# Performance work log

Measured on AMD Instinct MI355X. Metric: run time of the kernel, lower is better.

Reference implementation:

```python
import jax, jax.numpy as jnp
import numpy as np

# ---- constants (from init_kwargs / Config) ----
C = 10            # number of classes
P = 128           # fixed prototype capacity per class (masked)
GAMMA = 0.1
B_CONST = 10.0    # b
TAO = 1.0
BETA = 1.0
LAMBDA = 0.1
THRESHOLD = 40.0
EPS = 1e-6        # nn.PairwiseDistance eps (added to the difference)


def setup_inputs() -> dict:
    key = jax.random.key(0)
    k1, k2 = jax.random.split(key)
    features = jax.random.normal(k1, (8192, 512), dtype=jnp.float32)
    labels = jax.random.randint(k2, (8192,), 0, C, dtype=jnp.int32)
    return {"features": features, "labels": labels}


def _assign_prototypes(features, labels):
    """Sequential prototype assignment (faithful to assign_prototype).
    Fixed-capacity store: protos [C,P,D], counts [C,P], nproto [C]."""
    D = features.shape[1]
    protos = jnp.zeros((C, P, D), features.dtype)
    counts = jnp.zeros((C, P), jnp.int32)
    nproto = jnp.zeros((C,), jnp.int32)

    def step(carry, xs):
        protos, counts, nproto = carry
        f, l = xs
        row = protos[l]                       # [P, D]
        cnt = counts[l]                       # [P]
        n = nproto[l]
        valid = jnp.arange(P) < n
        d2 = jnp.sum((f[None, :] - row + EPS) ** 2, axis=-1)
        d2m = jnp.where(valid, d2, jnp.inf)
        idx = jnp.argmin(d2m)
        dmin = jnp.sqrt(d2m[idx])
        do_update = (n > 0) & (dmin < THRESHOLD)
        # running-mean update of closest prototype
        c = cnt[idx].astype(f.dtype)
        new_val = (row[idx] * c + f) / (c + 1.0)
        app_idx = jnp.minimum(n, P - 1)       # append slot (clamped; never hit with these settings)
        tgt_idx = jnp.where(do_update, idx, app_idx)
        tgt_val = jnp.where(do_update, new_val, f)
        tgt_cnt = jnp.where(do_update, cnt[idx] + 1, 1)
        row = row.at[tgt_idx].set(tgt_val)
        cnt = cnt.at[tgt_idx].set(tgt_cnt)
        n = jnp.where(do_update, n, jnp.minimum(n + 1, P))
        protos = protos.at[l].set(row)
        counts = counts.at[l].set(cnt)
        nproto = nproto.at[l].set(n)
        return (protos, counts, nproto), None

    (protos, counts, nproto), _ = jax.lax.scan(step, (protos, counts, nproto), (features, labels))
    return protos, nproto


def _forward(features, labels):
    # assign_prototype uses tensor(features).detach() -> stop_gradient
    protos, nproto = _assign_prototypes(jax.lax.stop_gradient(features), labels)
    B, D = features.shape
    flat = protos.reshape(C * P, D)
    valid = (jnp.arange(P)[None, :] < nproto[:, None]).reshape(C * P)

    # squared PairwiseDistance with eps added to the difference:
    # sum((f - p + eps)^2) = |f|^2 + |p|^2 - 2 f.p + 2*eps*(sum f - sum p) + D*eps^2
    f2 = jnp.sum(features ** 2, axis=-1)          # [B]
    p2 = jnp.sum(flat ** 2, axis=-1)              # [C*P]
    sf = jnp.sum(features, axis=-1)
    sp = jnp.sum(flat, axis=-1)
    d2 = (f2[:, None] + p2[None, :] - 2.0 * (features @ flat.T)
          + 2.0 * EPS * (sf[:, None] - sp[None, :]) + D * EPS * EPS)
    d2 = jnp.maximum(d2, 0.0)                     # [B, C*P]

    # dce loss: probability = 1e-6 + sum_label exp(-g d^2) / sum_all exp(-g d^2)
    expv = jnp.where(valid[None, :], jnp.exp(-GAMMA * d2), 0.0)
    per_class = expv.reshape(B, C, P).sum(-1)     # [B, C]
    one = per_class.sum(-1)                       # [B]
    num = jnp.take_along_axis(per_class, labels[:, None].astype(jnp.int32), axis=1)[:, 0]
    prob = 1e-6 + jnp.where(one > 0.0, num / one, one)
    dce_loss = jnp.sum(-jnp.log(prob))

    # pairwise loss: per sample, per existing class, min distance
    d2c = jnp.where(valid[None, :], d2, jnp.inf).reshape(B, C, P).min(-1)
    dmin = jnp.sqrt(d2c)                          # [B, C]
    sign = jnp.where(labels[:, None] == jnp.arange(C)[None, :], 1.0, -1.0)
    z = B_CONST - (TAO - dmin) * sign
    g = jnp.where(z > 10.0, z, jax.nn.softplus(BETA * z) / BETA)
    exists = nproto > 0                           # only classes present in all_prototypes
    pw_loss = jnp.sum(jnp.where(exists[None, :], g, 0.0))

    return dce_loss + LAMBDA * pw_loss


def reference(features, labels):
    return _forward(features, labels)
```

## Files before the change

### kernel.cpp

```cpp
#include <hip/hip_runtime.h>
#include <math.h>

#define NC 10
#define NP 128
#define ND 512
#define GAMMA  0.1f
#define BCONST 10.0f
#define TAO    1.0f
#define LAMBDA 0.1f
#define THR2   1600.0f
#define FEPS   1e-6f
#define NLDS   12
#define CH     16
#define WPB    4
#define NBLK   131

__device__ __forceinline__ float allredf(float v) {
#pragma unroll
  for (int m = 1; m < 64; m <<= 1) v += __shfl_xor(v, m, 64);
  return v;
}

__global__ __launch_bounds__(256)
void sumc_kernel(const float* __restrict__ feats, const int* __restrict__ labels, int B,
                 float* __restrict__ chunksum, int* __restrict__ order_g,
                 int* __restrict__ cb_g, int* __restrict__ cc_g, int* __restrict__ chb_g,
                 int* __restrict__ ncht_g, int* __restrict__ done_g,
                 int* __restrict__ fail_g, int* __restrict__ nproto_g,
                 float* __restrict__ out)
{
  __shared__ unsigned int lab32[2048];
  __shared__ int list[8192];
  __shared__ int wtot[4][NC];
  __shared__ int cb_s[NC], cc_s[NC], chb_s[NC];
  __shared__ int nchtot_s;

  const int t = threadIdx.x, lane = t & 63, w = t >> 6;

  const int4* lp = (const int4*)labels;
  for (int i = t; i < (B >> 2); i += 256) {
    int4 v = lp[i];
    lab32[i] = (unsigned)(v.x & 255) | ((unsigned)(v.y & 255) << 8)
             | ((unsigned)(v.z & 255) << 16) | ((unsigned)(v.w & 255) << 24);
  }
  __syncthreads();

  const int segsz = (B + 255) >> 8;
  const int i0 = t * segsz, i1 = min(i0 + segsz, B);

  int loc[NC];
#pragma unroll
  for (int c = 0; c < NC; ++c) loc[c] = 0;
  for (int i = i0; i < i1; ++i) {
    int l = (int)((lab32[i >> 2] >> ((i & 3) * 8)) & 255u);
#pragma unroll
    for (int c = 0; c < NC; ++c) loc[c] += (l == c);
  }
  int pre[NC];
#pragma unroll
  for (int c = 0; c < NC; ++c) pre[c] = loc[c];
#pragma unroll
  for (int m = 1; m < 64; m <<= 1) {
#pragma unroll
    for (int c = 0; c < NC; ++c) {
      int u = __shfl_up(pre[c], m, 64);
      if (lane >= m) pre[c] += u;
    }
  }
  if (lane == 63) {
#pragma unroll
    for (int c = 0; c < NC; ++c) wtot[w][c] = pre[c];
  }
  __syncthreads();

  int pos[NC];
  {
    int cb = 0, crun = 0;
#pragma unroll
    for (int c = 0; c < NC; ++c) {
      int tot = wtot[0][c] + wtot[1][c] + wtot[2][c] + wtot[3][c];
      int before = 0;
#pragma unroll
      for (int ww = 0; ww < 4; ++ww) before += (ww < w) ? wtot[ww][c] : 0;
      pos[c] = cb + before + (pre[c] - loc[c]);
      if (t == 0) { cb_s[c] = cb; cc_s[c] = tot; chb_s[c] = crun; }
      cb += tot;
      crun += (tot + CH - 1) / CH;
    }
    if (t == 0) nchtot_s = crun;
  }
  for (int i = i0; i < i1; ++i) {
    int l = (int)((lab32[i >> 2] >> ((i & 3) * 8)) & 255u);
#pragma unroll
    for (int c = 0; c < NC; ++c)
      if (l == c) list[pos[c]++] = i;
  }
  __syncthreads();

  if (blockIdx.x < 4) {
    int q = (B + 3) >> 2;
    int lo = blockIdx.x * q, hi = min(lo + q, B);
    for (int i = lo + t; i < hi; i += 256) order_g[i] = list[i];
  }
  if (blockIdx.x == 0) {
    if (t < NC) {
      cb_g[t] = cb_s[t]; cc_g[t] = cc_s[t]; chb_g[t] = chb_s[t];
      done_g[t] = 0; fail_g[t] = 0; nproto_g[t] = 0;
    }
    if (t == 0) { ncht_g[0] = nchtot_s; out[0] = 0.f; }
  }

  const int gwid = blockIdx.x * WPB + w;
  if (gwid >= nchtot_s) return;

  int c = 0;
  while (c + 1 < NC && chb_s[c + 1] <= gwid) ++c;
  const int g = gwid - chb_s[c];
  const int cnt = cc_s[c], base = cb_s[c];
  const int k0 = g * CH, k1 = min(k0 + CH, cnt);

  float S[8] = {0, 0, 0, 0, 0, 0, 0, 0};
  int k = k0;
  for (; k + 4 <= k1; k += 4) {
    float4 A[4], Bv[4];
#pragma unroll
    for (int j = 0; j < 4; ++j) {
      int idx = list[base + k + j];
      const float4* fp = (const float4*)(feats + (size_t)idx * ND + lane * 8);
      A[j] = fp[0]; Bv[j] = fp[1];
    }
#pragma unroll
    for (int j = 0; j < 4; ++j) {
      S[0]+=A[j].x; S[1]+=A[j].y; S[2]+=A[j].z; S[3]+=A[j].w;
      S[4]+=Bv[j].x; S[5]+=Bv[j].y; S[6]+=Bv[j].z; S[7]+=Bv[j].w;
    }
  }
  for (; k < k1; ++k) {
    int idx = list[base + k];
    const float4* fp = (const float4*)(feats + (size_t)idx * ND + lane * 8);
    float4 a = fp[0], b = fp[1];
    S[0]+=a.x; S[1]+=a.y; S[2]+=a.z; S[3]+=a.w;
    S[4]+=b.x; S[5]+=b.y; S[6]+=b.z; S[7]+=b.w;
  }
  float4* cp = (float4*)(chunksum + (size_t)gwid * ND + lane * 8);
  cp[0] = make_float4(S[0], S[1], S[2], S[3]);
  cp[1] = make_float4(S[4], S[5], S[6], S[7]);
}

__global__ __launch_bounds__(256)
void verify_kernel(const float* __restrict__ feats, int B,
                   const float* __restrict__ chunksum, const int* __restrict__ order_g,
                   const int* __restrict__ cb_g, const int* __restrict__ cc_g,
                   const int* __restrict__ chb_g, const int* __restrict__ ncht_g,
                   int* __restrict__ done_g, int* __restrict__ fail_g,
                   float* __restrict__ gproto, float* __restrict__ p2s,
                   float* __restrict__ sps, int* __restrict__ nproto_g)
{
  __shared__ int   cb_s[NC], cc_s[NC], chb_s[NC];
  __shared__ int   nchtot_s;
  __shared__ float ls_proto[NLDS][ND];
  __shared__ int   ls_cnt[NP];
  __shared__ int   fblock;

  const int t = threadIdx.x, lane = t & 63, w = t >> 6;
  if (t < NC) { cb_s[t] = cb_g[t]; cc_s[t] = cc_g[t]; chb_s[t] = chb_g[t]; }
  if (t == 32) nchtot_s = ncht_g[0];
  if (t == 33) fblock = 0;
  __syncthreads();

  const int gwid = blockIdx.x * WPB + w;
  if (gwid >= nchtot_s) return;

  int c = 0;
  while (c + 1 < NC && chb_s[c + 1] <= gwid) ++c;
  const int g = gwid - chb_s[c];
  const int cnt = cc_s[c], base = cb_s[c];
  const int nchc = (cnt + CH - 1) / CH;
  const int k0 = g * CH, k1 = min(k0 + CH, cnt);
  int myidx = (lane < CH && k0 + lane < cnt) ? order_g[base + k0 + lane] : 0;

  float P[8] = {0, 0, 0, 0, 0, 0, 0, 0};
  {
    const float* cbase = chunksum + (size_t)chb_s[c] * ND + lane * 8;
    int j = 0;
    for (; j + 4 <= g; j += 4) {
      float4 A[4], Bv[4];
#pragma unroll
      for (int q = 0; q < 4; ++q) {
        const float4* pp = (const float4*)(cbase + (size_t)(j + q) * ND);
        A[q] = pp[0]; Bv[q] = pp[1];
      }
#pragma unroll
      for (int q = 0; q < 4; ++q) {
        P[0]+=A[q].x; P[1]+=A[q].y; P[2]+=A[q].z; P[3]+=A[q].w;
        P[4]+=Bv[q].x; P[5]+=Bv[q].y; P[6]+=Bv[q].z; P[7]+=Bv[q].w;
      }
    }
    for (; j < g; ++j) {
      const float4* pp = (const float4*)(cbase + (size_t)j * ND);
      float4 a = pp[0], b = pp[1];
      P[0]+=a.x; P[1]+=a.y; P[2]+=a.z; P[3]+=a.w;
      P[4]+=b.x; P[5]+=b.y; P[6]+=b.z; P[7]+=b.w;
    }
  }

  int k = k0;
  for (; k + 4 <= k1; k += 4) {
    float4 A[4], Bv[4];
#pragma unroll
    for (int j = 0; j < 4; ++j) {
      int idx = __shfl(myidx, k + j - k0, 64);
      const float4* fp = (const float4*)(feats + (size_t)idx * ND + lane * 8);
      A[j] = fp[0]; Bv[j] = fp[1];
    }
    float part[4];
#pragma unroll
    for (int j = 0; j < 4; ++j) {
      int kk = k + j;
      float f[8] = {A[j].x, A[j].y, A[j].z, A[j].w, Bv[j].x, Bv[j].y, Bv[j].z, Bv[j].w};
      if (kk > 0) {
        float invk = 1.f / (float)kk;
        float p = 0.f;
#pragma unroll
        for (int e = 0; e < 8; ++e) { float d = f[e] - P[e] * invk + FEPS; p += d * d; }
        part[j] = p;
      } else part[j] = 0.f;
#pragma unroll
      for (int e = 0; e < 8; ++e) P[e] += f[e];
    }
#pragma unroll
    for (int m = 1; m < 64; m <<= 1) {
#pragma unroll
      for (int j = 0; j < 4; ++j) part[j] += __shfl_xor(part[j], m, 64);
    }
    if (lane == 0) {
#pragma unroll
      for (int j = 0; j < 4; ++j) {
        int kk = k + j;
        if (kk > 0 && !(part[j] < THR2)) atomicOr(&fail_g[c], 1);
      }
    }
  }
  for (; k < k1; ++k) {
    int idx = __shfl(myidx, k - k0, 64);
    const float4* fp = (const float4*)(feats + (size_t)idx * ND + lane * 8);
    float4 fa = fp[0], fb = fp[1];
    float f[8] = {fa.x, fa.y, fa.z, fa.w, fb.x, fb.y, fb.z, fb.w};
    if (k > 0) {
      float invk = 1.f / (float)k;
      float p = 0.f;
#pragma unroll
      for (int e = 0; e < 8; ++e) { float d = f[e] - P[e] * invk + FEPS; p += d * d; }
      float d2 = allredf(p);
      if (!(d2 < THR2) && lane == 0) atomicOr(&fail_g[c], 1);
    }
#pragma unroll
    for (int e = 0; e < 8; ++e) P[e] += f[e];
  }

  if (g == nchc - 1) {
    float invc = 1.f / (float)cnt;
    float p[8];
#pragma unroll
    for (int e = 0; e < 8; ++e) p[e] = P[e] * invc;
    float4* gp = (float4*)(gproto + (size_t)c * NP * ND + lane * 8);
    gp[0] = make_float4(p[0], p[1], p[2], p[3]);
    gp[1] = make_float4(p[4], p[5], p[6], p[7]);
    float P2p = 0.f, SPp = 0.f;
#pragma unroll
    for (int e = 0; e < 8; ++e) { P2p += p[e]*p[e]; SPp += p[e]; }
    float P2 = allredf(P2p), SP = allredf(SPp);
    if (lane == 0) { p2s[c*NP] = P2; sps[c*NP] = SP; nproto_g[c] = 1; }
  }

  __threadfence();
  int old = 0;
  if (lane == 0) old = atomicAdd(&done_g[c], 1);
  old = __shfl(old, 0, 64);
  if (old != nchc - 1) return;
  __threadfence();
  int fv = 0;
  if (lane == 0) fv = atomicOr(&fail_g[c], 0);
  fv = __shfl(fv, 0, 64);
  if (!fv) return;

  if (lane == 0) { while (atomicCAS(&fblock, 0, 1) != 0) {} }

  {
    float p0[8];
    int cnt0 = 0, n = 0;
    float fA[8], fB[8], fC[8];

    auto LOADF = [&](float (&buf)[8], int m) {
      int idx = order_g[base + m];
      const float4* fp = (const float4*)(feats + (size_t)idx * ND + lane * 8);
      float4 a = fp[0], b = fp[1];
      buf[0]=a.x; buf[1]=a.y; buf[2]=a.z; buf[3]=a.w;
      buf[4]=b.x; buf[5]=b.y; buf[6]=b.z; buf[7]=b.w;
    };
    auto STEP = [&](float (&f)[8]) {
      float best = 3.4e38f;
      int bidx = 0;
      if (n > 0) {
        float part = 0.f;
#pragma unroll
        for (int e = 0; e < 8; ++e) { float d = f[e] - p0[e] + FEPS; part += d * d; }
        best = allredf(part);
        for (int j = 1; j < n; ++j) {
          float pj[8];
          if (j <= NLDS) {
            const float4* pp = (const float4*)(&ls_proto[j-1][lane*8]);
            float4 a = pp[0], b = pp[1];
            pj[0]=a.x; pj[1]=a.y; pj[2]=a.z; pj[3]=a.w;
            pj[4]=b.x; pj[5]=b.y; pj[6]=b.z; pj[7]=b.w;
          } else {
            const float4* pp = (const float4*)(gproto + ((size_t)c*NP + j)*ND + lane*8);
            float4 a = pp[0], b = pp[1];
            pj[0]=a.x; pj[1]=a.y; pj[2]=a.z; pj[3]=a.w;
            pj[4]=b.x; pj[5]=b.y; pj[6]=b.z; pj[7]=b.w;
          }
          float part2 = 0.f;
#pragma unroll
          for (int e = 0; e < 8; ++e) { float d = f[e] - pj[e] + FEPS; part2 += d * d; }
          float tot = allredf(part2);
          if (tot < best) { best = tot; bidx = j; }
        }
      }
      if (n > 0 && best < THR2) {
        if (bidx == 0) {
          float cc = (float)cnt0, iv = 1.f / (cc + 1.f);
#pragma unroll
          for (int e = 0; e < 8; ++e) p0[e] = (p0[e]*cc + f[e]) * iv;
          cnt0++;
        } else {
          int ci = ls_cnt[bidx];
          float cc = (float)ci, iv = 1.f / (cc + 1.f);
          if (bidx <= NLDS) {
            float* row = &ls_proto[bidx-1][lane*8];
#pragma unroll
            for (int e = 0; e < 8; ++e) row[e] = (row[e]*cc + f[e]) * iv;
          } else {
            float* row = gproto + ((size_t)c*NP + bidx)*ND + lane*8;
#pragma unroll
            for (int e = 0; e < 8; ++e) row[e] = (row[e]*cc + f[e]) * iv;
          }
          if (lane == 0) ls_cnt[bidx] = ci + 1;
        }
      } else {
        int app = min(n, NP - 1);
        if (app == 0) {
#pragma unroll
          for (int e = 0; e < 8; ++e) p0[e] = f[e];
          cnt0 = 1;
        } else if (app <= NLDS) {
          float* row = &ls_proto[app-1][lane*8];
#pragma unroll
          for (int e = 0; e < 8; ++e) row[e] = f[e];
          if (lane == 0) ls_cnt[app] = 1;
        } else {
          float* row = gproto + ((size_t)c*NP + app)*ND + lane*8;
#pragma unroll
          for (int e = 0; e < 8; ++e) row[e] = f[e];
          if (lane == 0) ls_cnt[app] = 1;
        }
        n = min(n + 1, NP);
      }
    };

    if (cnt > 0) LOADF(fA, 0);
    if (cnt > 1) LOADF(fB, 1);
    if (cnt > 2) LOADF(fC, 2);
    int m = 0;
    while (m < cnt) {
      STEP(fA); ++m; if (m + 2 < cnt) LOADF(fA, m + 2);
      if (m >= cnt) break;
      STEP(fB); ++m; if (m + 2 < cnt) LOADF(fB, m + 2);
      if (m >= cnt) break;
      STEP(fC); ++m; if (m + 2 < cnt) LOADF(fC, m + 2);
    }

    for (int j = 0; j < n; ++j) {
      float pj[8];
      if (j == 0) {
#pragma unroll
        for (int e = 0; e < 8; ++e) pj[e] = p0[e];
      } else if (j <= NLDS) {
        const float4* pp = (const float4*)(&ls_proto[j-1][lane*8]);
        float4 a = pp[0], b = pp[1];
        pj[0]=a.x; pj[1]=a.y; pj[2]=a.z; pj[3]=a.w;
        pj[4]=b.x; pj[5]=b.y; pj[6]=b.z; pj[7]=b.w;
      } else {
        const float4* pp = (const float4*)(gproto + ((size_t)c*NP + j)*ND + lane*8);
        float4 a = pp[0], b = pp[1];
        pj[0]=a.x; pj[1]=a.y; pj[2]=a.z; pj[3]=a.w;
        pj[4]=b.x; pj[5]=b.y; pj[6]=b.z; pj[7]=b.w;
      }
      float4* gp = (float4*)(gproto + ((size_t)c*NP + j)*ND + lane*8);
      gp[0] = make_float4(pj[0], pj[1], pj[2], pj[3]);
      gp[1] = make_float4(pj[4], pj[5], pj[6], pj[7]);
      float P2p = 0.f, SPp = 0.f;
#pragma unroll
      for (int e = 0; e < 8; ++e) { P2p += pj[e]*pj[e]; SPp += pj[e]; }
      float P2 = allredf(P2p), SP = allredf(SPp);
      if (lane == 0) { p2s[c*NP + j] = P2; sps[c*NP + j] = SP; }
    }
    if (lane == 0) nproto_g[c] = n;
  }

  __threadfence_block();
  if (lane == 0) atomicExch(&fblock, 0);
}

__global__ __launch_bounds__(256)
void loss_kernel(const float* __restrict__ feats, const int* __restrict__ labels, int B,
                 const float* __restrict__ gproto, const float* __restrict__ p2s,
                 const float* __restrict__ sps, const int* __restrict__ nproto_g,
                 float* __restrict__ out)
{
  __shared__ float bsum[4];
  const int lane = threadIdx.x & 63;
  const int wid  = threadIdx.x >> 6;
  const int gw   = blockIdx.x * 4 + wid;
  const int nw   = gridDim.x * 4;

  int np[NC];
  bool fast = true;
#pragma unroll
  for (int cc = 0; cc < NC; ++cc) { np[cc] = nproto_g[cc]; fast &= (np[cc] == 1); }

  float acc = 0.f;
  if (fast) {
    float p2v[NC], spv[NC];
#pragma unroll
    for (int cc = 0; cc < NC; ++cc) { p2v[cc] = p2s[cc*NP]; spv[cc] = sps[cc*NP]; }
    for (int b = gw; b < B; b += nw) {
      const float4* fp = (const float4*)(feats + (size_t)b * ND + lane * 8);
      float4 a4 = fp[0], b4 = fp[1];
      float f[8] = {a4.x, a4.y, a4.z, a4.w, b4.x, b4.y, b4.z, b4.w};
      int lab = labels[b];
      float v[12];
#pragma unroll
      for (int cc = 0; cc < NC; ++cc) {
        const float4* pp = (const float4*)(gproto + (size_t)cc * NP * ND + lane * 8);
        float4 pa = pp[0], pb = pp[1];
        v[cc] = f[0]*pa.x + f[1]*pa.y + f[2]*pa.z + f[3]*pa.w
              + f[4]*pb.x + f[5]*pb.y + f[6]*pb.z + f[7]*pb.w;
      }
      float f2p = 0.f, sfp = 0.f;
#pragma unroll
      for (int e = 0; e < 8; ++e) { f2p += f[e]*f[e]; sfp += f[e]; }
      v[10] = f2p; v[11] = sfp;
#pragma unroll
      for (int m = 1; m < 64; m <<= 1) {
#pragma unroll
        for (int q = 0; q < 12; ++q) v[q] += __shfl_xor(v[q], m, 64);
      }
      float f2 = v[10], sf = v[11];
      float one = 0.f, num = 0.f, pw = 0.f;
#pragma unroll
      for (int cc = 0; cc < NC; ++cc) {
        float d2 = f2 + p2v[cc] - 2.f*v[cc]
                 + 2.f*FEPS*(sf - spv[cc]) + (float)ND*FEPS*FEPS;
        d2 = fmaxf(d2, 0.f);
        float e = expf(-GAMMA * d2);
        one += e;
        if (cc == lab) num = e;
        float dmin = sqrtf(d2);
        float sign = (cc == lab) ? 1.f : -1.f;
        float z = BCONST - (TAO - dmin) * sign;
        float gg = (z > 10.f) ? z : log1pf(expf(z));
        pw += gg;
      }
      float prob = 1e-6f + ((one > 0.f) ? num / one : one);
      acc += -logf(prob) + LAMBDA * pw;
    }
  } else {
    for (int b = gw; b < B; b += nw) {
      const float4* fp = (const float4*)(feats + (size_t)b * ND + lane * 8);
      float4 a4 = fp[0], b4 = fp[1];
      float f[8] = {a4.x, a4.y, a4.z, a4.w, b4.x, b4.y, b4.z, b4.w};
      float f2p = 0.f, sfp = 0.f;
#pragma unroll
      for (int e = 0; e < 8; ++e) { f2p += f[e]*f[e]; sfp += f[e]; }
      float f2 = allredf(f2p);
      float sf = allredf(sfp);
      int lab = labels[b];
      float one = 0.f, num = 0.f, pw = 0.f;
      for (int cc = 0; cc < NC; ++cc) {
        int nn = np[cc];
        if (nn <= 0) continue;
        float sume = 0.f, bestd2 = 3.4e38f;
        for (int j = 0; j < nn; ++j) {
          const float4* pp = (const float4*)(gproto + ((size_t)cc*NP + j)*ND + lane*8);
          float4 pa = pp[0], pb = pp[1];
          float dp = f[0]*pa.x + f[1]*pa.y + f[2]*pa.z + f[3]*pa.w
                   + f[4]*pb.x + f[5]*pb.y + f[6]*pb.z + f[7]*pb.w;
          float dot = allredf(dp);
          float d2 = f2 + p2s[cc*NP + j] - 2.f*dot
                   + 2.f*FEPS*(sf - sps[cc*NP + j]) + (float)ND*FEPS*FEPS;
          d2 = fmaxf(d2, 0.f);
          sume  += expf(-GAMMA * d2);
          bestd2 = fminf(bestd2, d2);
        }
        one += sume;
        if (cc == lab) num = sume;
        float dmin = sqrtf(bestd2);
        float sign = (cc == lab) ? 1.f : -1.f;
        float z = BCONST - (TAO - dmin) * sign;
        float g = (z > 10.f) ? z : log1pf(expf(z));
        pw += g;
      }
      float prob = 1e-6f + ((one > 0.f) ? num / one : one);
      acc += -logf(prob) + LAMBDA * pw;
    }
  }

  if (lane == 0) bsum[wid] = acc;
  __syncthreads();
  if (threadIdx.x == 0) atomicAdd(out, bsum[0] + bsum[1] + bsum[2] + bsum[3]);
}

extern "C" void kernel_launch(void* const* d_in, const int* in_sizes, int n_in,
                              void* d_out, int out_size, void* d_ws, size_t ws_size,
                              hipStream_t stream) {
  const float* feats  = (const float*)d_in[0];
  const int*   labels = (const int*)d_in[1];
  int B = in_sizes[0] / ND;
  const int maxwin = (B + CH - 1) / CH + NC;

  float* gproto   = (float*)d_ws;
  float* p2s      = gproto + (size_t)NC * NP * ND;
  float* sps      = p2s + NC * NP;
  float* chunksum = sps + NC * NP;
  int*   order_g  = (int*)(chunksum + (size_t)maxwin * ND);
  int*   cb_g     = order_g + B;
  int*   cc_g     = cb_g + NC;
  int*   chb_g    = cc_g + NC;
  int*   ncht_g   = chb_g + NC;
  int*   done_g   = ncht_g + 1;
  int*   fail_g   = done_g + NC;
  int*   nproto_g = fail_g + NC;
  float* outf     = (float*)d_out;

  hipLaunchKernelGGL(sumc_kernel, dim3(NBLK), dim3(256), 0, stream,
                     feats, labels, B, chunksum, order_g, cb_g, cc_g, chb_g,
                     ncht_g, done_g, fail_g, nproto_g, outf);
  hipLaunchKernelGGL(verify_kernel, dim3(NBLK), dim3(256), 0, stream,
                     feats, B, chunksum, order_g, cb_g, cc_g, chb_g, ncht_g,
                     done_g, fail_g, gproto, p2s, sps, nproto_g);
  hipLaunchKernelGGL(loss_kernel, dim3(2048), dim3(256), 0, stream,
                     feats, labels, B, gproto, p2s, sps, nproto_g, outf);
}
```

Measured before the change: 78.42 us.

## Fuse verify and loss kernels with a grid-wide completion barrier

```diff
diff --git a/kernel.cpp b/kernel.cpp
--- a/kernel.cpp
+++ b/kernel.cpp
@@ -27,7 +27,7 @@
                  int* __restrict__ cb_g, int* __restrict__ cc_g, int* __restrict__ chb_g,
                  int* __restrict__ ncht_g, int* __restrict__ done_g,
                  int* __restrict__ fail_g, int* __restrict__ nproto_g,
-                 float* __restrict__ out)
+                 int* __restrict__ cdone_g, float* __restrict__ out)
 {
   __shared__ unsigned int lab32[2048];
   __shared__ int list[8192];
@@ -107,7 +107,7 @@
       cb_g[t] = cb_s[t]; cc_g[t] = cc_s[t]; chb_g[t] = chb_s[t];
       done_g[t] = 0; fail_g[t] = 0; nproto_g[t] = 0;
     }
-    if (t == 0) { ncht_g[0] = nchtot_s; out[0] = 0.f; }
+    if (t == 0) { ncht_g[0] = nchtot_s; cdone_g[0] = 0; out[0] = 0.f; }
   }
 
   const int gwid = blockIdx.x * WPB + w;
@@ -148,167 +148,248 @@
 }
 
 __global__ __launch_bounds__(256)
-void verify_kernel(const float* __restrict__ feats, int B,
-                   const float* __restrict__ chunksum, const int* __restrict__ order_g,
-                   const int* __restrict__ cb_g, const int* __restrict__ cc_g,
-                   const int* __restrict__ chb_g, const int* __restrict__ ncht_g,
-                   int* __restrict__ done_g, int* __restrict__ fail_g,
-                   float* __restrict__ gproto, float* __restrict__ p2s,
-                   float* __restrict__ sps, int* __restrict__ nproto_g)
+void vloss_kernel(const float* __restrict__ feats, const int* __restrict__ labels, int B,
+                  const float* __restrict__ chunksum, const int* __restrict__ order_g,
+                  const int* __restrict__ cb_g, const int* __restrict__ cc_g,
+                  const int* __restrict__ chb_g, const int* __restrict__ ncht_g,
+                  int* __restrict__ done_g, int* __restrict__ fail_g,
+                  float* __restrict__ gproto, float* __restrict__ p2s,
+                  float* __restrict__ sps, int* __restrict__ nproto_g,
+                  int* __restrict__ cdone_g, float* __restrict__ out)
 {
   __shared__ int   cb_s[NC], cc_s[NC], chb_s[NC];
-  __shared__ int   nchtot_s;
+  __shared__ int   nchtot_s, target_s, fblock;
   __shared__ float ls_proto[NLDS][ND];
   __shared__ int   ls_cnt[NP];
-  __shared__ int   fblock;
+  __shared__ float bsum[4];
 
   const int t = threadIdx.x, lane = t & 63, w = t >> 6;
   if (t < NC) { cb_s[t] = cb_g[t]; cc_s[t] = cc_g[t]; chb_s[t] = chb_g[t]; }
   if (t == 32) nchtot_s = ncht_g[0];
   if (t == 33) fblock = 0;
   __syncthreads();
+  if (t == 0) {
+    int tg = 0;
+#pragma unroll
+    for (int c = 0; c < NC; ++c) tg += (cc_s[c] > 0);
+    target_s = tg;
+  }
+  __syncthreads();
 
   const int gwid = blockIdx.x * WPB + w;
-  if (gwid >= nchtot_s) return;
-
-  int c = 0;
-  while (c + 1 < NC && chb_s[c + 1] <= gwid) ++c;
-  const int g = gwid - chb_s[c];
-  const int cnt = cc_s[c], base = cb_s[c];
-  const int nchc = (cnt + CH - 1) / CH;
-  const int k0 = g * CH, k1 = min(k0 + CH, cnt);
-  int myidx = (lane < CH && k0 + lane < cnt) ? order_g[base + k0 + lane] : 0;
-
-  float P[8] = {0, 0, 0, 0, 0, 0, 0, 0};
-  {
-    const float* cbase = chunksum + (size_t)chb_s[c] * ND + lane * 8;
-    int j = 0;
-    for (; j + 4 <= g; j += 4) {
+
+  if (gwid < nchtot_s) {
+    int c = 0;
+    while (c + 1 < NC && chb_s[c + 1] <= gwid) ++c;
+    const int g = gwid - chb_s[c];
+    const int cnt = cc_s[c], base = cb_s[c];
+    const int nchc = (cnt + CH - 1) / CH;
+    const int k0 = g * CH, k1 = min(k0 + CH, cnt);
+    int myidx = (lane < CH && k0 + lane < cnt) ? order_g[base + k0 + lane] : 0;
+
+    float P[8] = {0, 0, 0, 0, 0, 0, 0, 0};
+    {
+      const float* cbase = chunksum + (size_t)chb_s[c] * ND + lane * 8;
+      int j = 0;
+      for (; j + 4 <= g; j += 4) {
+        float4 A[4], Bv[4];
+#pragma unroll
+        for (int q = 0; q < 4; ++q) {
+          const float4* pp = (const float4*)(cbase + (size_t)(j + q) * ND);
+          A[q] = pp[0]; Bv[q] = pp[1];
+        }
+#pragma unroll
+        for (int q = 0; q < 4; ++q) {
+          P[0]+=A[q].x; P[1]+=A[q].y; P[2]+=A[q].z; P[3]+=A[q].w;
+          P[4]+=Bv[q].x; P[5]+=Bv[q].y; P[6]+=Bv[q].z; P[7]+=Bv[q].w;
+        }
+      }
+      for (; j < g; ++j) {
+        const float4* pp = (const float4*)(cbase + (size_t)j * ND);
+        float4 a = pp[0], b = pp[1];
+        P[0]+=a.x; P[1]+=a.y; P[2]+=a.z; P[3]+=a.w;
+        P[4]+=b.x; P[5]+=b.y; P[6]+=b.z; P[7]+=b.w;
+      }
+    }
+
+    int k = k0;
+    for (; k + 4 <= k1; k += 4) {
       float4 A[4], Bv[4];
 #pragma unroll
-      for (int q = 0; q < 4; ++q) {
-        const float4* pp = (const float4*)(cbase + (size_t)(j + q) * ND);
-        A[q] = pp[0]; Bv[q] = pp[1];
-      }
-#pragma unroll
-      for (int q = 0; q < 4; ++q) {
-        P[0]+=A[q].x; P[1]+=A[q].y; P[2]+=A[q].z; P[3]+=A[q].w;
-        P[4]+=Bv[q].x; P[5]+=Bv[q].y; P[6]+=Bv[q].z; P[7]+=Bv[q].w;
-      }
-    }
-    for (; j < g; ++j) {
-      const float4* pp = (const float4*)(cbase + (size_t)j * ND);
-      float4 a = pp[0], b = pp[1];
-      P[0]+=a.x; P[1]+=a.y; P[2]+=a.z; P[3]+=a.w;
-      P[4]+=b.x; P[5]+=b.y; P[6]+=b.z; P[7]+=b.w;
-    }
-  }
-
-  int k = k0;
-  for (; k + 4 <= k1; k += 4) {
-    float4 A[4], Bv[4];
-#pragma unroll
-    for (int j = 0; j < 4; ++j) {
-      int idx = __shfl(myidx, k + j - k0, 64);
-      const float4* fp = (const float4*)(feats + (size_t)idx * ND + lane * 8);
-      A[j] = fp[0]; Bv[j] = fp[1];
-    }
-    float part[4];
-#pragma unroll
-    for (int j = 0; j < 4; ++j) {
-      int kk = k + j;
-      float f[8] = {A[j].x, A[j].y, A[j].z, A[j].w, Bv[j].x, Bv[j].y, Bv[j].z, Bv[j].w};
-      if (kk > 0) {
-        float invk = 1.f / (float)kk;
-        float p = 0.f;
-#pragma unroll
-        for (int e = 0; e < 8; ++e) { float d = f[e] - P[e] * invk + FEPS; p += d * d; }
-        part[j] = p;
-      } else part[j] = 0.f;
-#pragma unroll
-      for (int e = 0; e < 8; ++e) P[e] += f[e];
-    }
-#pragma unroll
-    for (int m = 1; m < 64; m <<= 1) {
-#pragma unroll
-      for (int j = 0; j < 4; ++j) part[j] += __shfl_xor(part[j], m, 64);
-    }
-    if (lane == 0) {
+      for (int j = 0; j < 4; ++j) {
+        int idx = __shfl(myidx, k + j - k0, 64);
+        const float4* fp = (const float4*)(feats + (size_t)idx * ND + lane * 8);
+        A[j] = fp[0]; Bv[j] = fp[1];
+      }
+      float part[4];
 #pragma unroll
       for (int j = 0; j < 4; ++j) {
         int kk = k + j;
-        if (kk > 0 && !(part[j] < THR2)) atomicOr(&fail_g[c], 1);
-      }
-    }
-  }
-  for (; k < k1; ++k) {
-    int idx = __shfl(myidx, k - k0, 64);
-    const float4* fp = (const float4*)(feats + (size_t)idx * ND + lane * 8);
-    float4 fa = fp[0], fb = fp[1];
-    float f[8] = {fa.x, fa.y, fa.z, fa.w, fb.x, fb.y, fb.z, fb.w};
-    if (k > 0) {
-      float invk = 1.f / (float)k;
-      float p = 0.f;
-#pragma unroll
-      for (int e = 0; e < 8; ++e) { float d = f[e] - P[e] * invk + FEPS; p += d * d; }
-      float d2 = allredf(p);
-      if (!(d2 < THR2) && lane == 0) atomicOr(&fail_g[c], 1);
-    }
-#pragma unroll
-    for (int e = 0; e < 8; ++e) P[e] += f[e];
-  }
-
-  if (g == nchc - 1) {
-    float invc = 1.f / (float)cnt;
-    float p[8];
-#pragma unroll
-    for (int e = 0; e < 8; ++e) p[e] = P[e] * invc;
-    float4* gp = (float4*)(gproto + (size_t)c * NP * ND + lane * 8);
-    gp[0] = make_float4(p[0], p[1], p[2], p[3]);
-    gp[1] = make_float4(p[4], p[5], p[6], p[7]);
-    float P2p = 0.f, SPp = 0.f;
-#pragma unroll
-    for (int e = 0; e < 8; ++e) { P2p += p[e]*p[e]; SPp += p[e]; }
-    float P2 = allredf(P2p), SP = allredf(SPp);
-    if (lane == 0) { p2s[c*NP] = P2; sps[c*NP] = SP; nproto_g[c] = 1; }
-  }
-
-  __threadfence();
-  int old = 0;
-  if (lane == 0) old = atomicAdd(&done_g[c], 1);
-  old = __shfl(old, 0, 64);
-  if (old != nchc - 1) return;
-  __threadfence();
-  int fv = 0;
-  if (lane == 0) fv = atomicOr(&fail_g[c], 0);
-  fv = __shfl(fv, 0, 64);
-  if (!fv) return;
-
-  if (lane == 0) { while (atomicCAS(&fblock, 0, 1) != 0) {} }
-
-  {
-    float p0[8];
-    int cnt0 = 0, n = 0;
-    float fA[8], fB[8], fC[8];
-
-    auto LOADF = [&](float (&buf)[8], int m) {
-      int idx = order_g[base + m];
+        float f[8] = {A[j].x, A[j].y, A[j].z, A[j].w, Bv[j].x, Bv[j].y, Bv[j].z, Bv[j].w};
+        if (kk > 0) {
+          float invk = 1.f / (float)kk;
+          float p = 0.f;
+#pragma unroll
+          for (int e = 0; e < 8; ++e) { float d = f[e] - P[e] * invk + FEPS; p += d * d; }
+          part[j] = p;
+        } else part[j] = 0.f;
+#pragma unroll
+        for (int e = 0; e < 8; ++e) P[e] += f[e];
+      }
+#pragma unroll
+      for (int m = 1; m < 64; m <<= 1) {
+#pragma unroll
+        for (int j = 0; j < 4; ++j) part[j] += __shfl_xor(part[j], m, 64);
+      }
+      if (lane == 0) {
+#pragma unroll
+        for (int j = 0; j < 4; ++j) {
+          int kk = k + j;
+          if (kk > 0 && !(part[j] < THR2)) atomicOr(&fail_g[c], 1);
+        }
+      }
+    }
+    for (; k < k1; ++k) {
+      int idx = __shfl(myidx, k - k0, 64);
       const float4* fp = (const float4*)(feats + (size_t)idx * ND + lane * 8);
-      float4 a = fp[0], b = fp[1];
-      buf[0]=a.x; buf[1]=a.y; buf[2]=a.z; buf[3]=a.w;
-      buf[4]=b.x; buf[5]=b.y; buf[6]=b.z; buf[7]=b.w;
-    };
-    auto STEP = [&](float (&f)[8]) {
-      float best = 3.4e38f;
-      int bidx = 0;
-      if (n > 0) {
-        float part = 0.f;
-#pragma unroll
-        for (int e = 0; e < 8; ++e) { float d = f[e] - p0[e] + FEPS; part += d * d; }
-        best = allredf(part);
-        for (int j = 1; j < n; ++j) {
+      float4 fa = fp[0], fb = fp[1];
+      float f[8] = {fa.x, fa.y, fa.z, fa.w, fb.x, fb.y, fb.z, fb.w};
+      if (k > 0) {
+        float invk = 1.f / (float)k;
+        float p = 0.f;
+#pragma unroll
+        for (int e = 0; e < 8; ++e) { float d = f[e] - P[e] * invk + FEPS; p += d * d; }
+        float d2 = allredf(p);
+        if (!(d2 < THR2) && lane == 0) atomicOr(&fail_g[c], 1);
+      }
+#pragma unroll
+      for (int e = 0; e < 8; ++e) P[e] += f[e];
+    }
+
+    if (g == nchc - 1) {
+      float invc = 1.f / (float)cnt;
+      float p[8];
+#pragma unroll
+      for (int e = 0; e < 8; ++e) p[e] = P[e] * invc;
+      float4* gp = (float4*)(gproto + (size_t)c * NP * ND + lane * 8);
+      gp[0] = make_float4(p[0], p[1], p[2], p[3]);
+      gp[1] = make_float4(p[4], p[5], p[6], p[7]);
+      float P2p = 0.f, SPp = 0.f;
+#pragma unroll
+      for (int e = 0; e < 8; ++e) { P2p += p[e]*p[e]; SPp += p[e]; }
+      float P2 = allredf(P2p), SP = allredf(SPp);
+      if (lane == 0) { p2s[c*NP] = P2; sps[c*NP] = SP; nproto_g[c] = 1; }
+    }
+
+    __threadfence();
+    int old = 0;
+    if (lane == 0)
+      old = __hip_atomic_fetch_add(&done_g[c], 1, __ATOMIC_ACQ_REL, __HIP_MEMORY_SCOPE_AGENT);
+    old = __shfl(old, 0, 64);
+    if (old == nchc - 1) {
+      int fv = 0;
+      if (lane == 0) fv = atomicOr(&fail_g[c], 0);
+      fv = __shfl(fv, 0, 64);
+      if (fv) {
+        if (lane == 0) { while (atomicCAS(&fblock, 0, 1) != 0) {} }
+        float p0[8];
+        int cnt0 = 0, n = 0;
+        float fA[8], fB[8], fC[8];
+
+        auto LOADF = [&](float (&buf)[8], int m) {
+          int idx = order_g[base + m];
+          const float4* fp = (const float4*)(feats + (size_t)idx * ND + lane * 8);
+          float4 a = fp[0], b = fp[1];
+          buf[0]=a.x; buf[1]=a.y; buf[2]=a.z; buf[3]=a.w;
+          buf[4]=b.x; buf[5]=b.y; buf[6]=b.z; buf[7]=b.w;
+        };
+        auto STEP = [&](float (&f)[8]) {
+          float best = 3.4e38f;
+          int bidx = 0;
+          if (n > 0) {
+            float part = 0.f;
+#pragma unroll
+            for (int e = 0; e < 8; ++e) { float d = f[e] - p0[e] + FEPS; part += d * d; }
+            best = allredf(part);
+            for (int j = 1; j < n; ++j) {
+              float pj[8];
+              if (j <= NLDS) {
+                const float4* pp = (const float4*)(&ls_proto[j-1][lane*8]);
+                float4 a = pp[0], b = pp[1];
+                pj[0]=a.x; pj[1]=a.y; pj[2]=a.z; pj[3]=a.w;
+                pj[4]=b.x; pj[5]=b.y; pj[6]=b.z; pj[7]=b.w;
+              } else {
+                const float4* pp = (const float4*)(gproto + ((size_t)c*NP + j)*ND + lane*8);
+                float4 a = pp[0], b = pp[1];
+                pj[0]=a.x; pj[1]=a.y; pj[2]=a.z; pj[3]=a.w;
+                pj[4]=b.x; pj[5]=b.y; pj[6]=b.z; pj[7]=b.w;
+              }
+              float part2 = 0.f;
+#pragma unroll
+              for (int e = 0; e < 8; ++e) { float d = f[e] - pj[e] + FEPS; part2 += d * d; }
+              float tot = allredf(part2);
+              if (tot < best) { best = tot; bidx = j; }
+            }
+          }
+          if (n > 0 && best < THR2) {
+            if (bidx == 0) {
+              float cc = (float)cnt0, iv = 1.f / (cc + 1.f);
+#pragma unroll
+              for (int e = 0; e < 8; ++e) p0[e] = (p0[e]*cc + f[e]) * iv;
+              cnt0++;
+            } else {
+              int ci = ls_cnt[bidx];
+              float cc = (float)ci, iv = 1.f / (cc + 1.f);
+              if (bidx <= NLDS) {
+                float* row = &ls_proto[bidx-1][lane*8];
+#pragma unroll
+                for (int e = 0; e < 8; ++e) row[e] = (row[e]*cc + f[e]) * iv;
+              } else {
+                float* row = gproto + ((size_t)c*NP + bidx)*ND + lane*8;
+#pragma unroll
+                for (int e = 0; e < 8; ++e) row[e] = (row[e]*cc + f[e]) * iv;
+              }
+              if (lane == 0) ls_cnt[bidx] = ci + 1;
+            }
+          } else {
+            int app = min(n, NP - 1);
+            if (app == 0) {
+#pragma unroll
+              for (int e = 0; e < 8; ++e) p0[e] = f[e];
+              cnt0 = 1;
+            } else if (app <= NLDS) {
+              float* row = &ls_proto[app-1][lane*8];
+#pragma unroll
+              for (int e = 0; e < 8; ++e) row[e] = f[e];
+              if (lane == 0) ls_cnt[app] = 1;
+            } else {
+              float* row = gproto + ((size_t)c*NP + app)*ND + lane*8;
+#pragma unroll
+              for (int e = 0; e < 8; ++e) row[e] = f[e];
+              if (lane == 0) ls_cnt[app] = 1;
+            }
+            n = min(n + 1, NP);
+          }
+        };
+
+        if (cnt > 0) LOADF(fA, 0);
+        if (cnt > 1) LOADF(fB, 1);
+        if (cnt > 2) LOADF(fC, 2);
+        int m = 0;
+        while (m < cnt) {
+          STEP(fA); ++m; if (m + 2 < cnt) LOADF(fA, m + 2);
+          if (m >= cnt) break;
+          STEP(fB); ++m; if (m + 2 < cnt) LOADF(fB, m + 2);
+          if (m >= cnt) break;
+          STEP(fC); ++m; if (m + 2 < cnt) LOADF(fC, m + 2);
+        }
+
+        for (int j = 0; j < n; ++j) {
           float pj[8];
-          if (j <= NLDS) {
+          if (j == 0) {
+#pragma unroll
+            for (int e = 0; e < 8; ++e) pj[e] = p0[e];
+          } else if (j <= NLDS) {
             const float4* pp = (const float4*)(&ls_proto[j-1][lane*8]);
             float4 a = pp[0], b = pp[1];
             pj[0]=a.x; pj[1]=a.y; pj[2]=a.z; pj[3]=a.w;
@@ -319,205 +400,127 @@
             pj[0]=a.x; pj[1]=a.y; pj[2]=a.z; pj[3]=a.w;
             pj[4]=b.x; pj[5]=b.y; pj[6]=b.z; pj[7]=b.w;
           }
-          float part2 = 0.f;
-#pragma unroll
-          for (int e = 0; e < 8; ++e) { float d = f[e] - pj[e] + FEPS; part2 += d * d; }
-          float tot = allredf(part2);
-          if (tot < best) { best = tot; bidx = j; }
-        }
-      }
-      if (n > 0 && best < THR2) {
-        if (bidx == 0) {
-          float cc = (float)cnt0, iv = 1.f / (cc + 1.f);
-#pragma unroll
-          for (int e = 0; e < 8; ++e) p0[e] = (p0[e]*cc + f[e]) * iv;
-          cnt0++;
-        } else {
-          int ci = ls_cnt[bidx];
-          float cc = (float)ci, iv = 1.f / (cc + 1.f);
-          if (bidx <= NLDS) {
-            float* row = &ls_proto[bidx-1][lane*8];
-#pragma unroll
-            for (int e = 0; e < 8; ++e) row[e] = (row[e]*cc + f[e]) * iv;
-          } else {
-            float* row = gproto + ((size_t)c*NP + bidx)*ND + lane*8;
-#pragma unroll
-            for (int e = 0; e < 8; ++e) row[e] = (row[e]*cc + f[e]) * iv;
+          float4* gp = (float4*)(gproto + ((size_t)c*NP + j)*ND + lane*8);
+          gp[0] = make_float4(pj[0], pj[1], pj[2], pj[3]);
+          gp[1] = make_float4(pj[4], pj[5], pj[6], pj[7]);
+          float P2p = 0.f, SPp = 0.f;
+#pragma unroll
+          for (int e = 0; e < 8; ++e) { P2p += pj[e]*pj[e]; SPp += pj[e]; }
+          float P2 = allredf(P2p), SP = allredf(SPp);
+          if (lane == 0) { p2s[c*NP + j] = P2; sps[c*NP + j] = SP; }
+        }
+        if (lane == 0) nproto_g[c] = n;
+        __threadfence_block();
+        if (lane == 0) atomicExch(&fblock, 0);
+      }
+      __threadfence();
+      if (lane == 0)
+        __hip_atomic_fetch_add(cdone_g, 1, __ATOMIC_RELEASE, __HIP_MEMORY_SCOPE_AGENT);
+    }
+  }
+
+  while (__hip_atomic_load(cdone_g, __ATOMIC_RELAXED, __HIP_MEMORY_SCOPE_AGENT) < target_s)
+    __builtin_amdgcn_s_sleep(1);
+  (void)__hip_atomic_load(cdone_g, __ATOMIC_ACQUIRE, __HIP_MEMORY_SCOPE_AGENT);
+
+  {
+    const int NWTOT = gridDim.x * WPB;
+    int np[NC];
+    bool fast = true;
+#pragma unroll
+    for (int cc = 0; cc < NC; ++cc) { np[cc] = nproto_g[cc]; fast &= (np[cc] == 1); }
+
+    float acc = 0.f;
+    if (fast) {
+      float p2v[NC], spv[NC];
+#pragma unroll
+      for (int cc = 0; cc < NC; ++cc) { p2v[cc] = p2s[cc*NP]; spv[cc] = sps[cc*NP]; }
+      for (int b = gwid; b < B; b += NWTOT) {
+        const float4* fp = (const float4*)(feats + (size_t)b * ND + lane * 8);
+        float4 a4 = fp[0], b4 = fp[1];
+        float f[8] = {a4.x, a4.y, a4.z, a4.w, b4.x, b4.y, b4.z, b4.w};
+        int lab = labels[b];
+        float v[12];
+#pragma unroll
+        for (int cc = 0; cc < NC; ++cc) {
+          const float4* pp = (const float4*)(gproto + (size_t)cc * NP * ND + lane * 8);
+          float4 pa = pp[0], pb = pp[1];
+          v[cc] = f[0]*pa.x + f[1]*pa.y + f[2]*pa.z + f[3]*pa.w
+                + f[4]*pb.x + f[5]*pb.y + f[6]*pb.z + f[7]*pb.w;
+        }
+        float f2p = 0.f, sfp = 0.f;
+#pragma unroll
+        for (int e = 0; e < 8; ++e) { f2p += f[e]*f[e]; sfp += f[e]; }
+        v[10] = f2p; v[11] = sfp;
+#pragma unroll
+        for (int m = 1; m < 64; m <<= 1) {
+#pragma unroll
+          for (int q = 0; q < 12; ++q) v[q] += __shfl_xor(v[q], m, 64);
+        }
+        float f2 = v[10], sf = v[11];
+        float one = 0.f, num = 0.f, pw = 0.f;
+#pragma unroll
+        for (int cc = 0; cc < NC; ++cc) {
+          float d2 = f2 + p2v[cc] - 2.f*v[cc]
+                   + 2.f*FEPS*(sf - spv[cc]) + (float)ND*FEPS*FEPS;
+          d2 = fmaxf(d2, 0.f);
+          float e = expf(-GAMMA * d2);
+          one += e;
+          if (cc == lab) num = e;
+          float dmin = sqrtf(d2);
+          float sign = (cc == lab) ? 1.f : -1.f;
+          float z = BCONST - (TAO - dmin) * sign;
+          float gg = (z > 10.f) ? z : log1pf(expf(z));
+          pw += gg;
+        }
+        float prob = 1e-6f + ((one > 0.f) ? num / one : one);
+        acc += -logf(prob) + LAMBDA * pw;
+      }
+    } else {
+      for (int b = gwid; b < B; b += NWTOT) {
+        const float4* fp = (const float4*)(feats + (size_t)b * ND + lane * 8);
+        float4 a4 = fp[0], b4 = fp[1];
+        float f[8] = {a4.x, a4.y, a4.z, a4.w, b4.x, b4.y, b4.z, b4.w};
+        float f2p = 0.f, sfp = 0.f;
+#pragma unroll
+        for (int e = 0; e < 8; ++e) { f2p += f[e]*f[e]; sfp += f[e]; }
+        float f2 = allredf(f2p);
+        float sf = allredf(sfp);
+        int lab = labels[b];
+        float one = 0.f, num = 0.f, pw = 0.f;
+        for (int cc = 0; cc < NC; ++cc) {
+          int nn = np[cc];
+          if (nn <= 0) continue;
+          float sume = 0.f, bestd2 = 3.4e38f;
+          for (int j = 0; j < nn; ++j) {
+            const float4* pp = (const float4*)(gproto + ((size_t)cc*NP + j)*ND + lane*8);
+            float4 pa = pp[0], pb = pp[1];
+            float dp = f[0]*pa.x + f[1]*pa.y + f[2]*pa.z + f[3]*pa.w
+                     + f[4]*pb.x + f[5]*pb.y + f[6]*pb.z + f[7]*pb.w;
+            float dot = allredf(dp);
+            float d2 = f2 + p2s[cc*NP + j] - 2.f*dot
+                     + 2.f*FEPS*(sf - sps[cc*NP + j]) + (float)ND*FEPS*FEPS;
+            d2 = fmaxf(d2, 0.f);
+            sume  += expf(-GAMMA * d2);
+            bestd2 = fminf(bestd2, d2);
           }
-          if (lane == 0) ls_cnt[bidx] = ci + 1;
-        }
-      } else {
-        int app = min(n, NP - 1);
-        if (app == 0) {
-#pragma unroll
-          for (int e = 0; e < 8; ++e) p0[e] = f[e];
-          cnt0 = 1;
-        } else if (app <= NLDS) {
-          float* row = &ls_proto[app-1][lane*8];
-#pragma unroll
-          for (int e = 0; e < 8; ++e) row[e] = f[e];
-          if (lane == 0) ls_cnt[app] = 1;
-        } else {
-          float* row = gproto + ((size_t)c*NP + app)*ND + lane*8;
-#pragma unroll
-          for (int e = 0; e < 8; ++e) row[e] = f[e];
-          if (lane == 0) ls_cnt[app] = 1;
-        }
-        n = min(n + 1, NP);
-      }
-    };
-
-    if (cnt > 0) LOADF(fA, 0);
-    if (cnt > 1) LOADF(fB, 1);
-    if (cnt > 2) LOADF(fC, 2);
-    int m = 0;
-    while (m < cnt) {
-      STEP(fA); ++m; if (m + 2 < cnt) LOADF(fA, m + 2);
-      if (m >= cnt) break;
-      STEP(fB); ++m; if (m + 2 < cnt) LOADF(fB, m + 2);
-      if (m >= cnt) break;
-      STEP(fC); ++m; if (m + 2 < cnt) LOADF(fC, m + 2);
-    }
-
-    for (int j = 0; j < n; ++j) {
-      float pj[8];
-      if (j == 0) {
-#pragma unroll
-        for (int e = 0; e < 8; ++e) pj[e] = p0[e];
-      } else if (j <= NLDS) {
-        const float4* pp = (const float4*)(&ls_proto[j-1][lane*8]);
-        float4 a = pp[0], b = pp[1];
-        pj[0]=a.x; pj[1]=a.y; pj[2]=a.z; pj[3]=a.w;
-        pj[4]=b.x; pj[5]=b.y; pj[6]=b.z; pj[7]=b.w;
-      } else {
-        const float4* pp = (const float4*)(gproto + ((size_t)c*NP + j)*ND + lane*8);
-        float4 a = pp[0], b = pp[1];
-        pj[0]=a.x; pj[1]=a.y; pj[2]=a.z; pj[3]=a.w;
-        pj[4]=b.x; pj[5]=b.y; pj[6]=b.z; pj[7]=b.w;
-      }
-      float4* gp = (float4*)(gproto + ((size_t)c*NP + j)*ND + lane*8);
-      gp[0] = make_float4(pj[0], pj[1], pj[2], pj[3]);
-      gp[1] = make_float4(pj[4], pj[5], pj[6], pj[7]);
-      float P2p = 0.f, SPp = 0.f;
-#pragma unroll
-      for (int e = 0; e < 8; ++e) { P2p += pj[e]*pj[e]; SPp += pj[e]; }
-      float P2 = allredf(P2p), SP = allredf(SPp);
-      if (lane == 0) { p2s[c*NP + j] = P2; sps[c*NP + j] = SP; }
-    }
-    if (lane == 0) nproto_g[c] = n;
-  }
-
-  __threadfence_block();
-  if (lane == 0) atomicExch(&fblock, 0);
-}
-
-__global__ __launch_bounds__(256)
-void loss_kernel(const float* __restrict__ feats, const int* __restrict__ labels, int B,
-                 const float* __restrict__ gproto, const float* __restrict__ p2s,
-                 const float* __restrict__ sps, const int* __restrict__ nproto_g,
-                 float* __restrict__ out)
-{
-  __shared__ float bsum[4];
-  const int lane = threadIdx.x & 63;
-  const int wid  = threadIdx.x >> 6;
-  const int gw   = blockIdx.x * 4 + wid;
-  const int nw   = gridDim.x * 4;
-
-  int np[NC];
-  bool fast = true;
-#pragma unroll
-  for (int cc = 0; cc < NC; ++cc) { np[cc] = nproto_g[cc]; fast &= (np[cc] == 1); }
-
-  float acc = 0.f;
-  if (fast) {
-    float p2v[NC], spv[NC];
-#pragma unroll
-    for (int cc = 0; cc < NC; ++cc) { p2v[cc] = p2s[cc*NP]; spv[cc] = sps[cc*NP]; }
-    for (int b = gw; b < B; b += nw) {
-      const float4* fp = (const float4*)(feats + (size_t)b * ND + lane * 8);
-      float4 a4 = fp[0], b4 = fp[1];
-      float f[8] = {a4.x, a4.y, a4.z, a4.w, b4.x, b4.y, b4.z, b4.w};
-      int lab = labels[b];
-      float v[12];
-#pragma unroll
-      for (int cc = 0; cc < NC; ++cc) {
-        const float4* pp = (const float4*)(gproto + (size_t)cc * NP * ND + lane * 8);
-        float4 pa = pp[0], pb = pp[1];
-        v[cc] = f[0]*pa.x + f[1]*pa.y + f[2]*pa.z + f[3]*pa.w
-              + f[4]*pb.x + f[5]*pb.y + f[6]*pb.z + f[7]*pb.w;
-      }
-      float f2p = 0.f, sfp = 0.f;
-#pragma unroll
-      for (int e = 0; e < 8; ++e) { f2p += f[e]*f[e]; sfp += f[e]; }
-      v[10] = f2p; v[11] = sfp;
-#pragma unroll
-      for (int m = 1; m < 64; m <<= 1) {
-#pragma unroll
-        for (int q = 0; q < 12; ++q) v[q] += __shfl_xor(v[q], m, 64);
-      }
-      float f2 = v[10], sf = v[11];
-      float one = 0.f, num = 0.f, pw = 0.f;
-#pragma unroll
-      for (int cc = 0; cc < NC; ++cc) {
-        float d2 = f2 + p2v[cc] - 2.f*v[cc]
-                 + 2.f*FEPS*(sf - spv[cc]) + (float)ND*FEPS*FEPS;
-        d2 = fmaxf(d2, 0.f);
-        float e = expf(-GAMMA * d2);
-        one += e;
-        if (cc == lab) num = e;
-        float dmin = sqrtf(d2);
-        float sign = (cc == lab) ? 1.f : -1.f;
-        float z = BCONST - (TAO - dmin) * sign;
-        float gg = (z > 10.f) ? z : log1pf(expf(z));
-        pw += gg;
-      }
-      float prob = 1e-6f + ((one > 0.f) ? num / one : one);
-      acc += -logf(prob) + LAMBDA * pw;
-    }
-  } else {
-    for (int b = gw; b < B; b += nw) {
-      const float4* fp = (const float4*)(feats + (size_t)b * ND + lane * 8);
-      float4 a4 = fp[0], b4 = fp[1];
-      float f[8] = {a4.x, a4.y, a4.z, a4.w, b4.x, b4.y, b4.z, b4.w};
-      float f2p = 0.f, sfp = 0.f;
-#pragma unroll
-      for (int e = 0; e < 8; ++e) { f2p += f[e]*f[e]; sfp += f[e]; }
-      float f2 = allredf(f2p);
-      float sf = allredf(sfp);
-      int lab = labels[b];
-      float one = 0.f, num = 0.f, pw = 0.f;
-      for (int cc = 0; cc < NC; ++cc) {
-        int nn = np[cc];
-        if (nn <= 0) continue;
-        float sume = 0.f, bestd2 = 3.4e38f;
-        for (int j = 0; j < nn; ++j) {
-          const float4* pp = (const float4*)(gproto + ((size_t)cc*NP + j)*ND + lane*8);
-          float4 pa = pp[0], pb = pp[1];
-          float dp = f[0]*pa.x + f[1]*pa.y + f[2]*pa.z + f[3]*pa.w
-                   + f[4]*pb.x + f[5]*pb.y + f[6]*pb.z + f[7]*pb.w;
-          float dot = allredf(dp);
-          float d2 = f2 + p2s[cc*NP + j] - 2.f*dot
-                   + 2.f*FEPS*(sf - sps[cc*NP + j]) + (float)ND*FEPS*FEPS;
-          d2 = fmaxf(d2, 0.f);
-          sume  += expf(-GAMMA * d2);
-          bestd2 = fminf(bestd2, d2);
-        }
-        one += sume;
-        if (cc == lab) num = sume;
-        float dmin = sqrtf(bestd2);
-        float sign = (cc == lab) ? 1.f : -1.f;
-        float z = BCONST - (TAO - dmin) * sign;
-        float g = (z > 10.f) ? z : log1pf(expf(z));
-        pw += g;
-      }
-      float prob = 1e-6f + ((one > 0.f) ? num / one : one);
-      acc += -logf(prob) + LAMBDA * pw;
-    }
-  }
-
-  if (lane == 0) bsum[wid] = acc;
-  __syncthreads();
-  if (threadIdx.x == 0) atomicAdd(out, bsum[0] + bsum[1] + bsum[2] + bsum[3]);
+          one += sume;
+          if (cc == lab) num = sume;
+          float dmin = sqrtf(bestd2);
+          float sign = (cc == lab) ? 1.f : -1.f;
+          float z = BCONST - (TAO - dmin) * sign;
+          float g = (z > 10.f) ? z : log1pf(expf(z));
+          pw += g;
+        }
+        float prob = 1e-6f + ((one > 0.f) ? num / one : one);
+        acc += -logf(prob) + LAMBDA * pw;
+      }
+    }
+
+    if (lane == 0) bsum[w] = acc;
+    __syncthreads();
+    if (t == 0) atomicAdd(out, bsum[0] + bsum[1] + bsum[2] + bsum[3]);
+  }
 }
 
 extern "C" void kernel_launch(void* const* d_in, const int* in_sizes, int n_in,
@@ -540,14 +543,14 @@
   int*   done_g   = ncht_g + 1;
   int*   fail_g   = done_g + NC;
   int*   nproto_g = fail_g + NC;
+  int*   cdone_g  = nproto_g + NC;
   float* outf     = (float*)d_out;
 
   hipLaunchKernelGGL(sumc_kernel, dim3(NBLK), dim3(256), 0, stream,
                      feats, labels, B, chunksum, order_g, cb_g, cc_g, chb_g,
-                     ncht_g, done_g, fail_g, nproto_g, outf);
-  hipLaunchKernelGGL(verify_kernel, dim3(NBLK), dim3(256), 0, stream,
-                     feats, B, chunksum, order_g, cb_g, cc_g, chb_g, ncht_g,
-                     done_g, fail_g, gproto, p2s, sps, nproto_g);
-  hipLaunchKernelGGL(loss_kernel, dim3(2048), dim3(256), 0, stream,
-                     feats, labels, B, gproto, p2s, sps, nproto_g, outf);
+                     ncht_g, done_g, fail_g, nproto_g, cdone_g, outf);
+  hipLaunchKernelGGL(vloss_kernel, dim3(NBLK), dim3(256), 0, stream,
+                     feats, labels, B, chunksum, order_g, cb_g, cc_g, chb_g,
+                     ncht_g, done_g, fail_g, gproto, p2s, sps, nproto_g,
+                     cdone_g, outf);
 }
```

Result: slower. 154.6 us (+97.2%).
